# Performance work log

Measured on AMD Instinct MI355X. Metric: run time of the kernel, lower is better.

## Reference

```python
import jax, jax.numpy as jnp
import numpy as np

B, E, H = 16384, 1024, 1024


def setup_inputs() -> dict:
    key = jax.random.key(0)
    ks = jax.random.split(key, 8)
    s = 1.0 / np.sqrt(H)
    return {
        "x": jax.random.normal(ks[0], (B, E), dtype=jnp.float32),
        "h": jax.random.normal(ks[1], (B, H), dtype=jnp.float32),
        "W_ri": jax.random.normal(ks[2], (E, H), dtype=jnp.float32) * s,
        "b_ri": jnp.zeros((H,), dtype=jnp.float32),
        "W_rh": jax.random.normal(ks[3], (H, H), dtype=jnp.float32) * s,
        "W_zi": jax.random.normal(ks[4], (E, H), dtype=jnp.float32) * s,
        "b_zi": jnp.zeros((H,), dtype=jnp.float32),
        "W_zh": jax.random.normal(ks[5], (H, H), dtype=jnp.float32) * s,
        "W_hi": jax.random.normal(ks[6], (E, H), dtype=jnp.float32) * s,
        "b_hi": jnp.zeros((H,), dtype=jnp.float32),
        "W_hh": jax.random.normal(ks[7], (H, H), dtype=jnp.float32) * s,
    }


def reference(x, h, W_ri, b_ri, W_rh, W_zi, b_zi, W_zh, W_hi, b_hi, W_hh):
    # GRU cell: r/z gates then candidate htilde, then blend.
    rt = jax.nn.sigmoid(x @ W_ri + b_ri + h @ W_rh)          # [B,H]
    zt = jax.nn.sigmoid(x @ W_zi + b_zi + h @ W_zh)          # [B,H]
    htilde = jnp.tanh(x @ W_hi + b_hi + (h * rt) @ W_hh)     # [B,H]
    h_new = (1.0 - zt) * h + zt * htilde                     # [B,H]
    # dp_keep_prob=1.0 -> dropout is identity; module returns (dropout(h), h)
    return h_new
```

## Files before the change

kernel.cpp:

```cpp
#include <hip/hip_runtime.h>


typedef short bf16x8 __attribute__((ext_vector_type(8)));
typedef float f32x4 __attribute__((ext_vector_type(4)));

template <int V> struct Ic { static constexpr int value = V; };

static __device__ __forceinline__ unsigned short f2bf(float f) {
    unsigned int u = __float_as_uint(f);
    return (unsigned short)((u + 0x7fffu + ((u >> 16) & 1u)) >> 16);
}
static __device__ __forceinline__ float bf2f(unsigned short s) {
    return __uint_as_float(((unsigned int)s) << 16);
}

__global__ void cast2_f32_bf16(const float* __restrict__ a,
                               const float* __restrict__ b,
                               unsigned short* __restrict__ da,
                               unsigned short* __restrict__ db, int n) {
    int i = (blockIdx.x * blockDim.x + threadIdx.x) * 4;
    const float* s;
    unsigned short* d;
    int off;
    if (i < n) { s = a; d = da; off = i; }
    else       { s = b; d = db; off = i - n; }
    float4 v = *(const float4*)(s + off);
    ushort4 o;
    o.x = f2bf(v.x); o.y = f2bf(v.y); o.z = f2bf(v.z); o.w = f2bf(v.w);
    *(ushort4*)(d + off) = o;
}

struct TPlan {
    const float* src[6];
    unsigned short* dst[6];
};
__global__ void transpose_cast6(TPlan p) {
    __shared__ float t[32][33];
    const float* src = p.src[blockIdx.z];
    unsigned short* dst = p.dst[blockIdx.z];
    int bx = blockIdx.x, by = blockIdx.y;
    int tx = threadIdx.x, ty = threadIdx.y;
#pragma unroll
    for (int i = 0; i < 4; ++i)
        t[ty + 8 * i][tx] = src[(by * 32 + ty + 8 * i) * 1024 + bx * 32 + tx];
    __syncthreads();
#pragma unroll
    for (int i = 0; i < 4; ++i) {
        int n = bx * 32 + ty + 8 * i;
        int k = by * 32 + tx;
        dst[n * 2048 + k] = f2bf(t[tx][ty + 8 * i]);
    }
}

template <int MODE, int NBN_LOG>
__global__ __launch_bounds__(512, 2) void gemm_gru(
        const unsigned short* __restrict__ Alo,
        const unsigned short* __restrict__ Ahi,
        const unsigned short* __restrict__ Bt,
        const float* __restrict__ bias_z,
        const float* __restrict__ bias_r,
        const unsigned short* __restrict__ hb,
        const unsigned short* __restrict__ ztb_in,
        const float* __restrict__ hf,
        unsigned short* __restrict__ ztb_out,
        unsigned short* __restrict__ ab_out,
        float* __restrict__ out) {
    constexpr int NBN = 1 << NBN_LOG;
    constexpr int NT = 32;
    __shared__ __attribute__((aligned(16))) short As[2][2][256 * 32];
    __shared__ __attribute__((aligned(16))) short Bs[2][2][256 * 32];

    const int t = threadIdx.x;
    const int lane = t & 63;
    const int wave = t >> 6;
    const int wm = wave >> 2, wn = wave & 3;

    const int i = blockIdx.x;
    const int bml = i & 7;
    const int bn = (i >> 3) & (NBN - 1);
    const int bmg = i >> (3 + NBN_LOG);
    const int bm = bmg * 8 + bml;

    const int l4 = lane & 15, kg = lane >> 4;
    const int rdcol = ((kg ^ ((l4 >> 1) & 3)) * 8);
    const int aoff = (wm * 128 + l4) * 32 + rdcol;
    const int boff = (wn * 64 + l4) * 32 + rdcol;

    const int srow = t >> 2;
    const int scol = (((t & 3) ^ ((t >> 3) & 3)) * 8);
    const int rowA0 = bm * 256;
    const int rowB0 = bn * 256;

    f32x4 acc[8][4] = {};
    bf16x8 bfr[4];

    auto stage_half = [&](const unsigned short* src, int stride, int grow0,
                          int kcol, short* dst) {
#pragma unroll
        for (int j = 0; j < 2; ++j) {
            const unsigned short* g =
                src + (size_t)(grow0 + j * 128 + srow) * stride + (kcol + scol);
            __builtin_amdgcn_global_load_lds(
                (const __attribute__((address_space(1))) void*)g,
                (__attribute__((address_space(3))) void*)(dst + (j * 512 + wave * 64) * 8),
                16, 0, 0);
        }
    };
    auto stage_A = [&](int T, int s) {
        const unsigned short* Ab = (T < 16) ? Alo : Ahi;
        stage_half(Ab, 1024, rowA0, ((T * 64) & 1023) + s * 32, &As[T & 1][s][0]);
    };
    auto stage_B = [&](int T, int s) {
        stage_half(Bt, 2048, rowB0, T * 64 + s * 32, &Bs[T & 1][s][0]);
    };

    auto nop = [] {};
    auto vm4 = [] { asm volatile("s_waitcnt vmcnt(4)" ::: "memory"); };
    auto vm0 = [] { asm volatile("s_waitcnt vmcnt(0)" ::: "memory"); };

    auto phase = [&](auto dC, auto mC, auto sC, auto stage, auto vmw) {
        constexpr int d = decltype(dC)::value;
        constexpr int m0 = decltype(mC)::value;
        constexpr int s = decltype(sC)::value;
        const short* Ab = &As[d][s][aoff];
        const short* Bb = &Bs[d][s][boff];
        bf16x8 af0 = *(const bf16x8*)(Ab + (m0 + 0) * 512);
        bf16x8 af1 = *(const bf16x8*)(Ab + (m0 + 1) * 512);
        bf16x8 af2 = *(const bf16x8*)(Ab + (m0 + 2) * 512);
        bf16x8 af3 = *(const bf16x8*)(Ab + (m0 + 3) * 512);
        if constexpr (m0 == 0) {
#pragma unroll
            for (int ni = 0; ni < 4; ++ni)
                bfr[ni] = *(const bf16x8*)(Bb + ni * 512);
        }
        stage();
        __builtin_amdgcn_s_barrier();
        asm volatile("s_waitcnt lgkmcnt(0)" ::: "memory");
        __builtin_amdgcn_s_setprio(1);
#pragma unroll
        for (int ni = 0; ni < 4; ++ni) {
            acc[m0 + 0][ni] = __builtin_amdgcn_mfma_f32_16x16x32_bf16(
                af0, bfr[ni], acc[m0 + 0][ni], 0, 0, 0);
            acc[m0 + 1][ni] = __builtin_amdgcn_mfma_f32_16x16x32_bf16(
                af1, bfr[ni], acc[m0 + 1][ni], 0, 0, 0);
        }
#pragma unroll
        for (int ni = 0; ni < 4; ++ni) {
            acc[m0 + 2][ni] = __builtin_amdgcn_mfma_f32_16x16x32_bf16(
                af2, bfr[ni], acc[m0 + 2][ni], 0, 0, 0);
            acc[m0 + 3][ni] = __builtin_amdgcn_mfma_f32_16x16x32_bf16(
                af3, bfr[ni], acc[m0 + 3][ni], 0, 0, 0);
        }
        __builtin_amdgcn_s_setprio(0);
        vmw();
        __builtin_amdgcn_s_barrier();
    };

    stage_A(0, 0); stage_B(0, 0); stage_A(0, 1); stage_B(0, 1);
    stage_A(1, 0); stage_B(1, 0);
    asm volatile("s_waitcnt vmcnt(4)" ::: "memory");
    __builtin_amdgcn_s_barrier();

    auto tile = [&](auto dC, int kt) {
        phase(dC, Ic<0>{}, Ic<0>{}, [&] { stage_A(kt + 1, 1); }, nop);
        phase(dC, Ic<4>{}, Ic<0>{}, [&] { stage_B(kt + 1, 1); }, vm4);
        phase(dC, Ic<0>{}, Ic<1>{}, [&] { stage_A(kt + 2, 0); }, nop);
        phase(dC, Ic<4>{}, Ic<1>{}, [&] { stage_B(kt + 2, 0); }, vm4);
    };

    for (int kt = 0; kt < NT - 2; kt += 2) {
        tile(Ic<0>{}, kt);
        tile(Ic<1>{}, kt + 1);
    }
    phase(Ic<0>{}, Ic<0>{}, Ic<0>{}, [&] { stage_A(NT - 1, 1); }, nop);
    phase(Ic<0>{}, Ic<4>{}, Ic<0>{}, [&] { stage_B(NT - 1, 1); }, vm4);
    phase(Ic<0>{}, Ic<0>{}, Ic<1>{}, nop, nop);
    phase(Ic<0>{}, Ic<4>{}, Ic<1>{}, nop, vm0);
    phase(Ic<1>{}, Ic<0>{}, Ic<0>{}, nop, nop);
    phase(Ic<1>{}, Ic<4>{}, Ic<0>{}, nop, nop);
    phase(Ic<1>{}, Ic<0>{}, Ic<1>{}, nop, nop);
    phase(Ic<1>{}, Ic<4>{}, Ic<1>{}, nop, nop);

    const int q4 = kg * 4;
#pragma unroll
    for (int mi = 0; mi < 8; ++mi) {
        int row0 = bm * 256 + wm * 128 + mi * 16 + q4;
#pragma unroll
        for (int ni = 0; ni < 4; ++ni) {
            int colg = bn * 256 + wn * 64 + ni * 16 + l4;
            if (MODE == 0) {
                bool isZ = colg < 1024;
                int col = colg & 1023;
                float bz = isZ ? bias_z[col] : bias_r[col];
#pragma unroll
                for (int r = 0; r < 4; ++r) {
                    int idx = (row0 + r) * 1024 + col;
                    float v = acc[mi][ni][r] + bz;
                    float s = 1.0f / (1.0f + __expf(-v));
                    if (isZ) ztb_out[idx] = f2bf(s);
                    else     ab_out[idx] = f2bf(bf2f(hb[idx]) * s);
                }
            } else {
                float bz = bias_z[colg];
#pragma unroll
                for (int r = 0; r < 4; ++r) {
                    int idx = (row0 + r) * 1024 + colg;
                    float v = acc[mi][ni][r] + bz;
                    float e = __expf(2.0f * v);
                    float ht = 1.0f - 2.0f / (e + 1.0f);
                    float hv = hf[idx];
                    float z = bf2f(ztb_in[idx]);
                    out[idx] = fmaf(z, ht - hv, hv);
                }
            }
        }
    }
}

extern "C" void kernel_launch(void* const* d_in, const int* in_sizes, int n_in,
                              void* d_out, int out_size, void* d_ws, size_t ws_size,
                              hipStream_t stream) {
    const float* x    = (const float*)d_in[0];
    const float* h    = (const float*)d_in[1];
    const float* W_ri = (const float*)d_in[2];
    const float* b_ri = (const float*)d_in[3];
    const float* W_rh = (const float*)d_in[4];
    const float* W_zi = (const float*)d_in[5];
    const float* b_zi = (const float*)d_in[6];
    const float* W_zh = (const float*)d_in[7];
    const float* W_hi = (const float*)d_in[8];
    const float* b_hi = (const float*)d_in[9];
    const float* W_hh = (const float*)d_in[10];
    float* out = (float*)d_out;

    const size_t MB = 1024ull * 1024ull;
    char* ws = (char*)d_ws;
    unsigned short* xb   = (unsigned short*)(ws);
    unsigned short* hb   = (unsigned short*)(ws + 32 * MB);
    unsigned short* ab   = (unsigned short*)(ws + 64 * MB);
    unsigned short* ztb  = (unsigned short*)(ws + 96 * MB);
    unsigned short* Bzr  = (unsigned short*)(ws + 128 * MB);
    unsigned short* Bh   = (unsigned short*)(ws + 136 * MB);

    const int NELEM = 16384 * 1024;
    cast2_f32_bf16<<<2 * NELEM / (256 * 4), 256, 0, stream>>>(x, h, xb, hb, NELEM);

    TPlan p;
    p.src[0] = W_zi; p.dst[0] = Bzr + 0 * 2048 + 0;
    p.src[1] = W_zh; p.dst[1] = Bzr + 0 * 2048 + 1024;
    p.src[2] = W_ri; p.dst[2] = Bzr + 1024 * 2048 + 0;
    p.src[3] = W_rh; p.dst[3] = Bzr + 1024 * 2048 + 1024;
    p.src[4] = W_hi; p.dst[4] = Bh + 0;
    p.src[5] = W_hh; p.dst[5] = Bh + 1024;
    transpose_cast6<<<dim3(32, 32, 6), dim3(32, 8), 0, stream>>>(p);

    gemm_gru<0, 3><<<512, 512, 0, stream>>>(xb, hb, Bzr, b_zi, b_ri,
                                            hb, nullptr, nullptr,
                                            ztb, ab, nullptr);
    gemm_gru<1, 2><<<256, 512, 0, stream>>>(xb, ab, Bh, b_hi, nullptr,
                                            nullptr, ztb, h,
                                            nullptr, nullptr, out);
}
```

Measured before the change: 466.2 us.

## Prefetch next phase's LDS fragments into double-buffered registers and drop barriers

Measured after the change: 472.4 us. About the same (+1.3%).

```diff
diff --git a/kernel.cpp b/kernel.cpp
--- a/kernel.cpp
+++ b/kernel.cpp
@@ -92,7 +92,8 @@
     const int rowB0 = bn * 256;
 
     f32x4 acc[8][4] = {};
-    bf16x8 bfr[4];
+    bf16x8 af[2][4];
+    bf16x8 bfr[2][4];
 
     auto stage_half = [&](const unsigned short* src, int stride, int grow0,
                           int kcol, short* dst) {
@@ -118,68 +119,108 @@
     auto vm4 = [] { asm volatile("s_waitcnt vmcnt(4)" ::: "memory"); };
     auto vm0 = [] { asm volatile("s_waitcnt vmcnt(0)" ::: "memory"); };
 
-    auto phase = [&](auto dC, auto mC, auto sC, auto stage, auto vmw) {
-        constexpr int d = decltype(dC)::value;
-        constexpr int m0 = decltype(mC)::value;
-        constexpr int s = decltype(sC)::value;
-        const short* Ab = &As[d][s][aoff];
-        const short* Bb = &Bs[d][s][boff];
-        bf16x8 af0 = *(const bf16x8*)(Ab + (m0 + 0) * 512);
-        bf16x8 af1 = *(const bf16x8*)(Ab + (m0 + 1) * 512);
-        bf16x8 af2 = *(const bf16x8*)(Ab + (m0 + 2) * 512);
-        bf16x8 af3 = *(const bf16x8*)(Ab + (m0 + 3) * 512);
-        if constexpr (m0 == 0) {
+    auto phase = [&](auto M0C, auto PAC, auto PBC, auto RKC, auto RDC,
+                     auto RSC, auto RMC, auto RAC, auto RBC, auto stage,
+                     auto vmw, auto barC) {
+        constexpr int m0 = decltype(M0C)::value;
+        constexpr int pa = decltype(PAC)::value;
+        constexpr int pb = decltype(PBC)::value;
+        constexpr int rk = decltype(RKC)::value;
+        constexpr int rd = decltype(RDC)::value;
+        constexpr int rs = decltype(RSC)::value;
+        constexpr int rm = decltype(RMC)::value;
+        constexpr int ra = decltype(RAC)::value;
+        constexpr int rb = decltype(RBC)::value;
+        stage();
+        if constexpr (rk >= 4) {
+            const short* Ab = &As[rd][rs][aoff];
+            af[ra][0] = *(const bf16x8*)(Ab + (rm + 0) * 512);
+            af[ra][1] = *(const bf16x8*)(Ab + (rm + 1) * 512);
+            af[ra][2] = *(const bf16x8*)(Ab + (rm + 2) * 512);
+            af[ra][3] = *(const bf16x8*)(Ab + (rm + 3) * 512);
+        }
+        if constexpr (rk == 8) {
+            const short* Bb = &Bs[rd][rs][boff];
 #pragma unroll
             for (int ni = 0; ni < 4; ++ni)
-                bfr[ni] = *(const bf16x8*)(Bb + ni * 512);
-        }
-        stage();
-        __builtin_amdgcn_s_barrier();
-        asm volatile("s_waitcnt lgkmcnt(0)" ::: "memory");
+                bfr[rb][ni] = *(const bf16x8*)(Bb + ni * 512);
+        }
+        if constexpr (rk == 8)
+            asm volatile("s_waitcnt lgkmcnt(8)" ::: "memory");
+        else if constexpr (rk == 4)
+            asm volatile("s_waitcnt lgkmcnt(4)" ::: "memory");
+        else
+            asm volatile("s_waitcnt lgkmcnt(0)" ::: "memory");
+        __builtin_amdgcn_sched_barrier(0);
         __builtin_amdgcn_s_setprio(1);
 #pragma unroll
         for (int ni = 0; ni < 4; ++ni) {
             acc[m0 + 0][ni] = __builtin_amdgcn_mfma_f32_16x16x32_bf16(
-                af0, bfr[ni], acc[m0 + 0][ni], 0, 0, 0);
+                af[pa][0], bfr[pb][ni], acc[m0 + 0][ni], 0, 0, 0);
             acc[m0 + 1][ni] = __builtin_amdgcn_mfma_f32_16x16x32_bf16(
-                af1, bfr[ni], acc[m0 + 1][ni], 0, 0, 0);
+                af[pa][1], bfr[pb][ni], acc[m0 + 1][ni], 0, 0, 0);
         }
 #pragma unroll
         for (int ni = 0; ni < 4; ++ni) {
             acc[m0 + 2][ni] = __builtin_amdgcn_mfma_f32_16x16x32_bf16(
-                af2, bfr[ni], acc[m0 + 2][ni], 0, 0, 0);
+                af[pa][2], bfr[pb][ni], acc[m0 + 2][ni], 0, 0, 0);
             acc[m0 + 3][ni] = __builtin_amdgcn_mfma_f32_16x16x32_bf16(
-                af3, bfr[ni], acc[m0 + 3][ni], 0, 0, 0);
+                af[pa][3], bfr[pb][ni], acc[m0 + 3][ni], 0, 0, 0);
         }
         __builtin_amdgcn_s_setprio(0);
         vmw();
-        __builtin_amdgcn_s_barrier();
+        if constexpr (decltype(barC)::value) __builtin_amdgcn_s_barrier();
     };
 
     stage_A(0, 0); stage_B(0, 0); stage_A(0, 1); stage_B(0, 1);
     stage_A(1, 0); stage_B(1, 0);
     asm volatile("s_waitcnt vmcnt(4)" ::: "memory");
     __builtin_amdgcn_s_barrier();
-
-    auto tile = [&](auto dC, int kt) {
-        phase(dC, Ic<0>{}, Ic<0>{}, [&] { stage_A(kt + 1, 1); }, nop);
-        phase(dC, Ic<4>{}, Ic<0>{}, [&] { stage_B(kt + 1, 1); }, vm4);
-        phase(dC, Ic<0>{}, Ic<1>{}, [&] { stage_A(kt + 2, 0); }, nop);
-        phase(dC, Ic<4>{}, Ic<1>{}, [&] { stage_B(kt + 2, 0); }, vm4);
+    {
+        const short* Ab = &As[0][0][aoff];
+        af[0][0] = *(const bf16x8*)(Ab + 0 * 512);
+        af[0][1] = *(const bf16x8*)(Ab + 1 * 512);
+        af[0][2] = *(const bf16x8*)(Ab + 2 * 512);
+        af[0][3] = *(const bf16x8*)(Ab + 3 * 512);
+        const short* Bb = &Bs[0][0][boff];
+#pragma unroll
+        for (int ni = 0; ni < 4; ++ni)
+            bfr[0][ni] = *(const bf16x8*)(Bb + ni * 512);
+    }
+
+    auto tileF = [&](auto dC, int kt, bool last2) {
+        constexpr int d = decltype(dC)::value;
+        phase(Ic<0>{}, Ic<0>{}, Ic<0>{}, Ic<4>{}, Ic<d>{}, Ic<0>{}, Ic<4>{},
+              Ic<1>{}, Ic<0>{}, [&] { stage_A(kt + 1, 1); }, nop, Ic<0>{});
+        phase(Ic<4>{}, Ic<1>{}, Ic<0>{}, Ic<8>{}, Ic<d>{}, Ic<1>{}, Ic<0>{},
+              Ic<0>{}, Ic<1>{}, [&] { stage_B(kt + 1, 1); }, vm4, Ic<1>{});
+        if (!last2) {
+            phase(Ic<0>{}, Ic<0>{}, Ic<1>{}, Ic<4>{}, Ic<d>{}, Ic<1>{}, Ic<4>{},
+                  Ic<1>{}, Ic<0>{}, [&] { stage_A(kt + 2, 0); }, nop, Ic<0>{});
+            phase(Ic<4>{}, Ic<1>{}, Ic<1>{}, Ic<8>{}, Ic<d ^ 1>{}, Ic<0>{},
+                  Ic<0>{}, Ic<0>{}, Ic<0>{}, [&] { stage_B(kt + 2, 0); }, vm4,
+                  Ic<1>{});
+        } else {
+            phase(Ic<0>{}, Ic<0>{}, Ic<1>{}, Ic<4>{}, Ic<d>{}, Ic<1>{}, Ic<4>{},
+                  Ic<1>{}, Ic<0>{}, nop, nop, Ic<0>{});
+            phase(Ic<4>{}, Ic<1>{}, Ic<1>{}, Ic<8>{}, Ic<d ^ 1>{}, Ic<0>{},
+                  Ic<0>{}, Ic<0>{}, Ic<0>{}, nop, vm0, Ic<1>{});
+        }
     };
 
     for (int kt = 0; kt < NT - 2; kt += 2) {
-        tile(Ic<0>{}, kt);
-        tile(Ic<1>{}, kt + 1);
+        tileF(Ic<0>{}, kt, false);
+        tileF(Ic<1>{}, kt + 1, false);
     }
-    phase(Ic<0>{}, Ic<0>{}, Ic<0>{}, [&] { stage_A(NT - 1, 1); }, nop);
-    phase(Ic<0>{}, Ic<4>{}, Ic<0>{}, [&] { stage_B(NT - 1, 1); }, vm4);
-    phase(Ic<0>{}, Ic<0>{}, Ic<1>{}, nop, nop);
-    phase(Ic<0>{}, Ic<4>{}, Ic<1>{}, nop, vm0);
-    phase(Ic<1>{}, Ic<0>{}, Ic<0>{}, nop, nop);
-    phase(Ic<1>{}, Ic<4>{}, Ic<0>{}, nop, nop);
-    phase(Ic<1>{}, Ic<0>{}, Ic<1>{}, nop, nop);
-    phase(Ic<1>{}, Ic<4>{}, Ic<1>{}, nop, nop);
+    tileF(Ic<0>{}, NT - 2, true);
+    phase(Ic<0>{}, Ic<0>{}, Ic<0>{}, Ic<4>{}, Ic<1>{}, Ic<0>{}, Ic<4>{},
+          Ic<1>{}, Ic<0>{}, nop, nop, Ic<0>{});
+    phase(Ic<4>{}, Ic<1>{}, Ic<0>{}, Ic<8>{}, Ic<1>{}, Ic<1>{}, Ic<0>{},
+          Ic<0>{}, Ic<1>{}, nop, nop, Ic<0>{});
+    phase(Ic<0>{}, Ic<0>{}, Ic<1>{}, Ic<4>{}, Ic<1>{}, Ic<1>{}, Ic<4>{},
+          Ic<1>{}, Ic<0>{}, nop, nop, Ic<0>{});
+    phase(Ic<4>{}, Ic<1>{}, Ic<1>{}, Ic<0>{}, Ic<0>{}, Ic<0>{}, Ic<0>{},
+          Ic<0>{}, Ic<0>{}, nop, nop, Ic<0>{});
 
     const int q4 = kg * 4;
 #pragma unroll
```

## Restructure GEMM LDS layout into row-halves with 64-wide K and finer phase schedule

Applied to the files above, without the earlier changes.

Result: slower. 485.7 us (+4.2%).

```diff
diff --git a/kernel.cpp b/kernel.cpp
--- a/kernel.cpp
+++ b/kernel.cpp
@@ -67,8 +67,8 @@
         float* __restrict__ out) {
     constexpr int NBN = 1 << NBN_LOG;
     constexpr int NT = 32;
-    __shared__ __attribute__((aligned(16))) short As[2][2][256 * 32];
-    __shared__ __attribute__((aligned(16))) short Bs[2][2][256 * 32];
+    __shared__ __attribute__((aligned(16))) short As[2][2][128 * 64];
+    __shared__ __attribute__((aligned(16))) short Bs[2][2][128 * 64];
 
     const int t = threadIdx.x;
     const int lane = t & 63;
@@ -82,104 +82,121 @@
     const int bm = bmg * 8 + bml;
 
     const int l4 = lane & 15, kg = lane >> 4;
-    const int rdcol = ((kg ^ ((l4 >> 1) & 3)) * 8);
-    const int aoff = (wm * 128 + l4) * 32 + rdcol;
-    const int boff = (wn * 64 + l4) * 32 + rdcol;
-
-    const int srow = t >> 2;
-    const int scol = (((t & 3) ^ ((t >> 3) & 3)) * 8);
+    const int cs0 = ((kg) ^ (l4 & 7)) * 8;
+    const int cs1 = ((4 + kg) ^ (l4 & 7)) * 8;
+    const short* aB[2] = { &As[0][wm][l4 * 64], &As[1][wm][l4 * 64] };
+    const short* bB[2] = { &Bs[0][wn >> 1][((wn & 1) * 64 + l4) * 64],
+                           &Bs[1][wn >> 1][((wn & 1) * 64 + l4) * 64] };
+
+    const int srow = t >> 3;
+    const int schunk = (((t & 7) ^ ((t >> 3) & 7)) * 8);
     const int rowA0 = bm * 256;
     const int rowB0 = bn * 256;
 
     f32x4 acc[8][4] = {};
-    bf16x8 bfr[4];
+    bf16x8 a[2][4];
+    bf16x8 bq[2][2][2];
 
     auto stage_half = [&](const unsigned short* src, int stride, int grow0,
                           int kcol, short* dst) {
 #pragma unroll
         for (int j = 0; j < 2; ++j) {
             const unsigned short* g =
-                src + (size_t)(grow0 + j * 128 + srow) * stride + (kcol + scol);
+                src + (size_t)(grow0 + j * 64 + srow) * stride + (kcol + schunk);
             __builtin_amdgcn_global_load_lds(
                 (const __attribute__((address_space(1))) void*)g,
                 (__attribute__((address_space(3))) void*)(dst + (j * 512 + wave * 64) * 8),
                 16, 0, 0);
         }
     };
-    auto stage_A = [&](int T, int s) {
+    auto stA = [&](int T, int h, short* dst) {
         const unsigned short* Ab = (T < 16) ? Alo : Ahi;
-        stage_half(Ab, 1024, rowA0, ((T * 64) & 1023) + s * 32, &As[T & 1][s][0]);
-    };
-    auto stage_B = [&](int T, int s) {
-        stage_half(Bt, 2048, rowB0, T * 64 + s * 32, &Bs[T & 1][s][0]);
+        stage_half(Ab, 1024, rowA0 + h * 128, (T * 64) & 1023, dst);
+    };
+    auto stB = [&](int T, int h, short* dst) {
+        stage_half(Bt, 2048, rowB0 + h * 128, T * 64, dst);
     };
 
     auto nop = [] {};
-    auto vm4 = [] { asm volatile("s_waitcnt vmcnt(4)" ::: "memory"); };
+    auto vm6 = [] { asm volatile("s_waitcnt vmcnt(6)" ::: "memory"); };
     auto vm0 = [] { asm volatile("s_waitcnt vmcnt(0)" ::: "memory"); };
 
-    auto phase = [&](auto dC, auto mC, auto sC, auto stage, auto vmw) {
-        constexpr int d = decltype(dC)::value;
-        constexpr int m0 = decltype(mC)::value;
-        constexpr int s = decltype(sC)::value;
-        const short* Ab = &As[d][s][aoff];
-        const short* Bb = &Bs[d][s][boff];
-        bf16x8 af0 = *(const bf16x8*)(Ab + (m0 + 0) * 512);
-        bf16x8 af1 = *(const bf16x8*)(Ab + (m0 + 1) * 512);
-        bf16x8 af2 = *(const bf16x8*)(Ab + (m0 + 2) * 512);
-        bf16x8 af3 = *(const bf16x8*)(Ab + (m0 + 3) * 512);
-        if constexpr (m0 == 0) {
-#pragma unroll
-            for (int ni = 0; ni < 4; ++ni)
-                bfr[ni] = *(const bf16x8*)(Bb + ni * 512);
+    auto phase = [&](auto TPc, auto MHc, auto NHc, auto RAc, auto RBc,
+                     auto stage, auto vmw) {
+        constexpr int TP = decltype(TPc)::value;
+        constexpr int MH = decltype(MHc)::value;
+        constexpr int NH = decltype(NHc)::value;
+        constexpr int RA = decltype(RAc)::value;
+        constexpr int RB = decltype(RBc)::value;
+        if constexpr (RA) {
+#pragma unroll
+            for (int m = 0; m < 4; ++m) {
+                a[0][m] = *(const bf16x8*)(aB[TP] + (MH * 64 + m * 16) * 64 + cs0);
+                a[1][m] = *(const bf16x8*)(aB[TP] + (MH * 64 + m * 16) * 64 + cs1);
+            }
+        }
+        if constexpr (RB) {
+#pragma unroll
+            for (int n = 0; n < 2; ++n) {
+                bq[NH][0][n] = *(const bf16x8*)(bB[TP] + (NH * 32 + n * 16) * 64 + cs0);
+                bq[NH][1][n] = *(const bf16x8*)(bB[TP] + (NH * 32 + n * 16) * 64 + cs1);
+            }
         }
         stage();
+        if constexpr (RA && RB)
+            asm volatile("s_waitcnt lgkmcnt(8)" ::: "memory");
         __builtin_amdgcn_s_barrier();
         asm volatile("s_waitcnt lgkmcnt(0)" ::: "memory");
+        __builtin_amdgcn_sched_barrier(0);
         __builtin_amdgcn_s_setprio(1);
 #pragma unroll
-        for (int ni = 0; ni < 4; ++ni) {
-            acc[m0 + 0][ni] = __builtin_amdgcn_mfma_f32_16x16x32_bf16(
-                af0, bfr[ni], acc[m0 + 0][ni], 0, 0, 0);
-            acc[m0 + 1][ni] = __builtin_amdgcn_mfma_f32_16x16x32_bf16(
-                af1, bfr[ni], acc[m0 + 1][ni], 0, 0, 0);
-        }
-#pragma unroll
-        for (int ni = 0; ni < 4; ++ni) {
-            acc[m0 + 2][ni] = __builtin_amdgcn_mfma_f32_16x16x32_bf16(
-                af2, bfr[ni], acc[m0 + 2][ni], 0, 0, 0);
-            acc[m0 + 3][ni] = __builtin_amdgcn_mfma_f32_16x16x32_bf16(
-                af3, bfr[ni], acc[m0 + 3][ni], 0, 0, 0);
-        }
+        for (int kk = 0; kk < 2; ++kk)
+#pragma unroll
+            for (int m = 0; m < 4; ++m)
+#pragma unroll
+                for (int n = 0; n < 2; ++n)
+                    acc[MH * 4 + m][NH * 2 + n] =
+                        __builtin_amdgcn_mfma_f32_16x16x32_bf16(
+                            a[kk][m], bq[NH][kk][n],
+                            acc[MH * 4 + m][NH * 2 + n], 0, 0, 0);
         __builtin_amdgcn_s_setprio(0);
         vmw();
         __builtin_amdgcn_s_barrier();
     };
 
-    stage_A(0, 0); stage_B(0, 0); stage_A(0, 1); stage_B(0, 1);
-    stage_A(1, 0); stage_B(1, 0);
-    asm volatile("s_waitcnt vmcnt(4)" ::: "memory");
+    stA(0, 0, &As[0][0][0]); stA(0, 1, &As[0][1][0]);
+    stB(0, 0, &Bs[0][0][0]); stB(0, 1, &Bs[0][1][0]);
+    stA(1, 0, &As[1][0][0]);
+    stB(1, 0, &Bs[1][0][0]); stB(1, 1, &Bs[1][1][0]);
+    asm volatile("s_waitcnt vmcnt(6)" ::: "memory");
     __builtin_amdgcn_s_barrier();
 
-    auto tile = [&](auto dC, int kt) {
-        phase(dC, Ic<0>{}, Ic<0>{}, [&] { stage_A(kt + 1, 1); }, nop);
-        phase(dC, Ic<4>{}, Ic<0>{}, [&] { stage_B(kt + 1, 1); }, vm4);
-        phase(dC, Ic<0>{}, Ic<1>{}, [&] { stage_A(kt + 2, 0); }, nop);
-        phase(dC, Ic<4>{}, Ic<1>{}, [&] { stage_B(kt + 2, 0); }, vm4);
-    };
-
-    for (int kt = 0; kt < NT - 2; kt += 2) {
-        tile(Ic<0>{}, kt);
-        tile(Ic<1>{}, kt + 1);
+    for (int I = 0; I < 15; ++I) {
+        const int To = 2 * I + 1, T2 = 2 * I + 2, T3 = 2 * I + 3;
+        phase(Ic<0>{}, Ic<0>{}, Ic<0>{}, Ic<1>{}, Ic<1>{},
+              [&] { stA(To, 1, &As[1][1][0]); }, nop);
+        phase(Ic<0>{}, Ic<0>{}, Ic<1>{}, Ic<0>{}, Ic<1>{}, nop, nop);
+        phase(Ic<0>{}, Ic<1>{}, Ic<0>{}, Ic<1>{}, Ic<0>{},
+              [&] { stB(T2, 0, &Bs[0][0][0]); }, nop);
+        phase(Ic<0>{}, Ic<1>{}, Ic<1>{}, Ic<0>{}, Ic<0>{},
+              [&] { stB(T2, 1, &Bs[0][1][0]); stA(T2, 0, &As[0][0][0]); }, vm6);
+        phase(Ic<1>{}, Ic<0>{}, Ic<0>{}, Ic<1>{}, Ic<1>{},
+              [&] { stA(T2, 1, &As[0][1][0]); }, nop);
+        phase(Ic<1>{}, Ic<0>{}, Ic<1>{}, Ic<0>{}, Ic<1>{}, nop, nop);
+        phase(Ic<1>{}, Ic<1>{}, Ic<0>{}, Ic<1>{}, Ic<0>{},
+              [&] { stB(T3, 0, &Bs[1][0][0]); }, nop);
+        phase(Ic<1>{}, Ic<1>{}, Ic<1>{}, Ic<0>{}, Ic<0>{},
+              [&] { stB(T3, 1, &Bs[1][1][0]); stA(T3, 0, &As[1][0][0]); }, vm6);
     }
-    phase(Ic<0>{}, Ic<0>{}, Ic<0>{}, [&] { stage_A(NT - 1, 1); }, nop);
-    phase(Ic<0>{}, Ic<4>{}, Ic<0>{}, [&] { stage_B(NT - 1, 1); }, vm4);
-    phase(Ic<0>{}, Ic<0>{}, Ic<1>{}, nop, nop);
-    phase(Ic<0>{}, Ic<4>{}, Ic<1>{}, nop, vm0);
-    phase(Ic<1>{}, Ic<0>{}, Ic<0>{}, nop, nop);
-    phase(Ic<1>{}, Ic<4>{}, Ic<0>{}, nop, nop);
-    phase(Ic<1>{}, Ic<0>{}, Ic<1>{}, nop, nop);
-    phase(Ic<1>{}, Ic<4>{}, Ic<1>{}, nop, nop);
+    phase(Ic<0>{}, Ic<0>{}, Ic<0>{}, Ic<1>{}, Ic<1>{},
+          [&] { stA(31, 1, &As[1][1][0]); }, nop);
+    phase(Ic<0>{}, Ic<0>{}, Ic<1>{}, Ic<0>{}, Ic<1>{}, nop, nop);
+    phase(Ic<0>{}, Ic<1>{}, Ic<0>{}, Ic<1>{}, Ic<0>{}, nop, nop);
+    phase(Ic<0>{}, Ic<1>{}, Ic<1>{}, Ic<0>{}, Ic<0>{}, nop, vm0);
+    phase(Ic<1>{}, Ic<0>{}, Ic<0>{}, Ic<1>{}, Ic<1>{}, nop, nop);
+    phase(Ic<1>{}, Ic<0>{}, Ic<1>{}, Ic<0>{}, Ic<1>{}, nop, nop);
+    phase(Ic<1>{}, Ic<1>{}, Ic<0>{}, Ic<1>{}, Ic<0>{}, nop, nop);
+    phase(Ic<1>{}, Ic<1>{}, Ic<1>{}, Ic<0>{}, Ic<0>{}, nop, nop);
 
     const int q4 = kg * 4;
 #pragma unroll
```
